# Kernel tuning notes

Measured on AMD Instinct MI355X. Metric: run time of the kernel, lower is better.

Reference implementation:

```python
import jax, jax.numpy as jnp
import numpy as np

L, B, N, D, K = 32, 4, 1000, 128, 8


def setup_inputs() -> dict:
    key = jax.random.key(0)
    ks = jax.random.split(key, 10)
    w = lambda k, s: (jax.random.normal(k, s, jnp.float32) * 0.05)
    return {
        "x": jax.random.normal(ks[0], (L, B, N, D), jnp.float32),
        "route_neighbors": jax.random.randint(ks[1], (N, K), 0, N),
        "t_in_w": w(ks[2], (3 * D, D)),
        "t_in_b": w(ks[3], (3 * D,)),
        "t_out_w": w(ks[4], (D, D)),
        "t_out_b": w(ks[5], (D,)),
        "s_in_w": w(ks[6], (3 * D, D)),
        "s_in_b": w(ks[7], (3 * D,)),
        "s_out_w": w(ks[8], (D, D)),
        "s_out_b": w(ks[9], (D,)),
        "n_heads": 8,
    }


def reference(x, route_neighbors, t_in_w, t_in_b, t_out_w, t_out_b,
              s_in_w, s_in_b, s_out_w, s_out_b, n_heads):
    l, b, n, d = x.shape
    h = n_heads
    dh = d // h
    scale = 1.0 / jnp.sqrt(jnp.asarray(dh, x.dtype))

    # ---- temporal MHA: attend over time axis L, batch = (B, N) ----
    wq, wk, wv = jnp.split(t_in_w, 3, axis=0)
    bq, bk, bv = jnp.split(t_in_b, 3, axis=0)
    q = (x @ wq.T + bq).reshape(l, b, n, h, dh)
    k = (x @ wk.T + bk).reshape(l, b, n, h, dh)
    v = (x @ wv.T + bv).reshape(l, b, n, h, dh)
    scores = jnp.einsum('lbnhd,mbnhd->bnhlm', q, k) * scale
    attn = jax.nn.softmax(scores, axis=-1)
    o = jnp.einsum('bnhlm,mbnhd->lbnhd', attn, v).reshape(l, b, n, d)
    t_out = o @ t_out_w.T + t_out_b

    # ---- spatial MHA: per node, single-token query over K gathered neighbors ----
    swq, swk, swv = jnp.split(s_in_w, 3, axis=0)
    sbq, sbk, sbv = jnp.split(s_in_b, 3, axis=0)
    xn = x[:, :, route_neighbors]                         # (L,B,N,K,D) gather
    sq = (x @ swq.T + sbq).reshape(l, b, n, h, dh)
    sk = (xn @ swk.T + sbk).reshape(l, b, n, -1, h, dh)
    sv = (xn @ swv.T + sbv).reshape(l, b, n, -1, h, dh)
    s_scores = jnp.einsum('lbnhd,lbnkhd->lbnhk', sq, sk) * scale
    s_attn = jax.nn.softmax(s_scores, axis=-1)
    so = jnp.einsum('lbnhk,lbnkhd->lbnhd', s_attn, sv).reshape(l, b, n, d)
    s_out = so @ s_out_w.T + s_out_b

    return t_out + s_out
```

## Files before the change

### kernel.cpp

```cpp
#include <hip/hip_runtime.h>
#include <math.h>

#define L_ 32
#define B_ 4
#define N_ 1000
#define D_ 128
#define H_ 8
#define DH_ 16
#define KN_ 8
#define M_ (L_ * B_ * N_)

typedef __attribute__((ext_vector_type(8))) short short8;
typedef __attribute__((ext_vector_type(8))) unsigned short ushort8v;
typedef __attribute__((ext_vector_type(4))) float floatx4;

static __device__ __forceinline__ unsigned short f2bf(float f) {
  union { float f; unsigned u; } v; v.f = f;
  unsigned r = v.u + 0x7fffu + ((v.u >> 16) & 1u);
  return (unsigned short)(r >> 16);
}
static __device__ __forceinline__ float bf2f(unsigned short s) {
  union { unsigned u; float f; } v; v.u = ((unsigned)s) << 16;
  return v.f;
}
static __device__ __forceinline__ void gload_lds16(const unsigned short* g,
                                                   unsigned short* l) {
  __builtin_amdgcn_global_load_lds(
      (const __attribute__((address_space(1))) unsigned int*)g,
      (__attribute__((address_space(3))) unsigned int*)l, 16, 0, 0);
}

__global__ __launch_bounds__(256) void prep_kernel(
    const float* __restrict__ x, const float* __restrict__ wt_in,
    const float* __restrict__ ws_in, const float* __restrict__ wt_out,
    const float* __restrict__ ws_out, unsigned short* __restrict__ ximg,
    unsigned short* __restrict__ wimg) {
  const int bid = blockIdx.x, t = threadIdx.x;
  const float* src;
  unsigned short* dst;
  if (bid < 1000) {
    src = x + (size_t)bid * 16384;
    dst = ximg + (size_t)bid * 16384;
  } else {
    int w = bid - 1000;
    if (w < 3) src = wt_in + (size_t)w * 16384;
    else if (w < 6) src = ws_in + (size_t)(w - 3) * 16384;
    else if (w == 6) src = wt_out;
    else src = ws_out;
    dst = wimg + (size_t)w * 16384;
  }
#pragma unroll
  for (int it = 0; it < 8; ++it) {
    int gi = it * 256 + t;
    int m = gi >> 4, g = gi & 15;
    const float4* sp = (const float4*)(src + m * 128 + g * 8);
    float4 a = sp[0], b = sp[1];
    ushort8v o;
    o[0] = f2bf(a.x); o[1] = f2bf(a.y); o[2] = f2bf(a.z); o[3] = f2bf(a.w);
    o[4] = f2bf(b.x); o[5] = f2bf(b.y); o[6] = f2bf(b.z); o[7] = f2bf(b.w);
    *(ushort8v*)(dst + (size_t)(m * 16 + (g ^ (m & 7))) * 8) = o;
  }
}

__global__ __launch_bounds__(256) void proj_mfma(
    const unsigned short* __restrict__ ximg,
    const unsigned short* __restrict__ wimg, const float* __restrict__ bias,
    unsigned short* __restrict__ out) {
  __shared__ unsigned short As[128 * 128];
  __shared__ unsigned short Bs[128 * 128];
  const int t = threadIdx.x;
  const int bm = blockIdx.x / 3, bn = blockIdx.x % 3;
  const unsigned short* aSrc = ximg + (size_t)bm * 16384;
  const unsigned short* bSrc = wimg + (size_t)bn * 16384;
#pragma unroll
  for (int it = 0; it < 8; ++it) {
    int gi = it * 256 + t;
    gload_lds16(aSrc + (size_t)gi * 8, &As[gi * 8]);
    gload_lds16(bSrc + (size_t)gi * 8, &Bs[gi * 8]);
  }
  __syncthreads();
  const int wave = t >> 6, lane = t & 63;
  const int wm = (wave >> 1) * 64, wn = (wave & 1) * 64;
  const int lq = lane >> 4, l16 = lane & 15;
  floatx4 acc[4][4] = {};
#pragma unroll
  for (int kk = 0; kk < 4; ++kk) {
    int g = kk * 4 + lq;
    short8 a[4], b[4];
#pragma unroll
    for (int i = 0; i < 4; ++i) {
      int ma = wm + i * 16 + l16;
      a[i] = *(const short8*)(&As[(ma * 16 + (g ^ (ma & 7))) * 8]);
      int nb = wn + i * 16 + l16;
      b[i] = *(const short8*)(&Bs[(nb * 16 + (g ^ (nb & 7))) * 8]);
    }
#pragma unroll
    for (int i = 0; i < 4; ++i)
#pragma unroll
      for (int j = 0; j < 4; ++j)
        acc[i][j] = __builtin_amdgcn_mfma_f32_16x16x32_bf16(a[i], b[j],
                                                            acc[i][j], 0, 0, 0);
  }
  const size_t rowBase = (size_t)bm * 128 + wm;
  const int colBase = bn * 128 + wn;
#pragma unroll
  for (int j = 0; j < 4; ++j) {
    float bb = bias[colBase + j * 16 + l16];
#pragma unroll
    for (int i = 0; i < 4; ++i) {
#pragma unroll
      for (int r = 0; r < 4; ++r) {
        size_t row = rowBase + i * 16 + lq * 4 + r;
        out[row * 384 + colBase + j * 16 + l16] = f2bf(acc[i][j][r] + bb);
      }
    }
  }
}

__global__ __launch_bounds__(256) void tattn_kernel(
    const unsigned short* __restrict__ qkv, unsigned short* __restrict__ oimg) {
  __shared__ unsigned short S[1536 * 8];
  const int t = threadIdx.x;
  const int b = blockIdx.x / N_;
  const int n = blockIdx.x % N_;
  const size_t rowStride = (size_t)B_ * N_ * 384;
  const unsigned short* gbase = qkv + ((size_t)b * N_ + n) * 384;
#pragma unroll
  for (int r = 0; r < 3; ++r) {
#pragma unroll
    for (int it = 0; it < 2; ++it) {
      const int s = it * 256 + t;
      const int m = s >> 4, g = s & 15;
      gload_lds16(gbase + (size_t)m * rowStride + r * 128 + (g ^ (m & 7)) * 8,
                  &S[(r * 512 + s) * 8]);
    }
  }
  asm volatile("s_waitcnt vmcnt(0)" ::: "memory");
  __syncthreads();

  const int wv = t >> 6, lane = t & 63;
  const int lq = lane >> 4, l16 = lane & 15;
  unsigned short* ob[8];
  int rsw[8];
#pragma unroll
  for (int lt = 0; lt < 2; ++lt)
#pragma unroll
    for (int r = 0; r < 4; ++r) {
      const int l = lt * 16 + lq * 4 + r;
      const size_t rg = ((size_t)l * B_ + b) * N_ + n;
      ob[lt * 4 + r] = oimg + (rg >> 7) * 16384 + (size_t)(rg & 127) * 128;
      rsw[lt * 4 + r] = (int)(rg & 7);
    }

#pragma unroll
  for (int hh = 0; hh < 2; ++hh) {
    const int h = wv * 2 + hh;
    short8 ka0 = {}, ka1 = {}, qb0 = {}, qb1 = {};
    if (lq < 2) {
      const int g = 2 * h + lq;
      const int m0 = l16, m1 = 16 + l16;
      ka0 = *(const short8*)&S[(512 + m0 * 16 + (g ^ (m0 & 7))) * 8];
      ka1 = *(const short8*)&S[(512 + m1 * 16 + (g ^ (m1 & 7))) * 8];
      qb0 = *(const short8*)&S[(m0 * 16 + (g ^ (m0 & 7))) * 8];
      qb1 = *(const short8*)&S[(m1 * 16 + (g ^ (m1 & 7))) * 8];
    }
    floatx4 st00 = {}, st01 = {}, st10 = {}, st11 = {};
    st00 = __builtin_amdgcn_mfma_f32_16x16x32_bf16(ka0, qb0, st00, 0, 0, 0);
    st01 = __builtin_amdgcn_mfma_f32_16x16x32_bf16(ka0, qb1, st01, 0, 0, 0);
    st10 = __builtin_amdgcn_mfma_f32_16x16x32_bf16(ka1, qb0, st10, 0, 0, 0);
    st11 = __builtin_amdgcn_mfma_f32_16x16x32_bf16(ka1, qb1, st11, 0, 0, 0);
    const int d = h * 16 + l16;
    const int gd = d >> 3, de = d & 7;
    short8 vb;
#pragma unroll
    for (int j = 0; j < 8; ++j) {
      const int m = ((j >> 2) << 4) + lq * 4 + (j & 3);
      vb[j] = (short)S[(1024 + m * 16 + (gd ^ (m & 7))) * 8 + de];
    }
    short8 pa0, pa1;
    {
      floatx4 a = st00 * 0.25f, c = st10 * 0.25f;
      float mx = fmaxf(fmaxf(fmaxf(a[0], a[1]), fmaxf(a[2], a[3])),
                       fmaxf(fmaxf(c[0], c[1]), fmaxf(c[2], c[3])));
      mx = fmaxf(mx, __shfl_xor(mx, 16));
      mx = fmaxf(mx, __shfl_xor(mx, 32));
      float p0 = __expf(a[0] - mx), p1 = __expf(a[1] - mx);
      float p2 = __expf(a[2] - mx), p3 = __expf(a[3] - mx);
      float p4 = __expf(c[0] - mx), p5 = __expf(c[1] - mx);
      float p6 = __expf(c[2] - mx), p7 = __expf(c[3] - mx);
      float sm = ((p0 + p1) + (p2 + p3)) + ((p4 + p5) + (p6 + p7));
      sm += __shfl_xor(sm, 16);
      sm += __shfl_xor(sm, 32);
      float inv = 1.f / sm;
      pa0[0] = (short)f2bf(p0 * inv); pa0[1] = (short)f2bf(p1 * inv);
      pa0[2] = (short)f2bf(p2 * inv); pa0[3] = (short)f2bf(p3 * inv);
      pa0[4] = (short)f2bf(p4 * inv); pa0[5] = (short)f2bf(p5 * inv);
      pa0[6] = (short)f2bf(p6 * inv); pa0[7] = (short)f2bf(p7 * inv);
    }
    {
      floatx4 a = st01 * 0.25f, c = st11 * 0.25f;
      float mx = fmaxf(fmaxf(fmaxf(a[0], a[1]), fmaxf(a[2], a[3])),
                       fmaxf(fmaxf(c[0], c[1]), fmaxf(c[2], c[3])));
      mx = fmaxf(mx, __shfl_xor(mx, 16));
      mx = fmaxf(mx, __shfl_xor(mx, 32));
      float p0 = __expf(a[0] - mx), p1 = __expf(a[1] - mx);
      float p2 = __expf(a[2] - mx), p3 = __expf(a[3] - mx);
      float p4 = __expf(c[0] - mx), p5 = __expf(c[1] - mx);
      float p6 = __expf(c[2] - mx), p7 = __expf(c[3] - mx);
      float sm = ((p0 + p1) + (p2 + p3)) + ((p4 + p5) + (p6 + p7));
      sm += __shfl_xor(sm, 16);
      sm += __shfl_xor(sm, 32);
      float inv = 1.f / sm;
      pa1[0] = (short)f2bf(p0 * inv); pa1[1] = (short)f2bf(p1 * inv);
      pa1[2] = (short)f2bf(p2 * inv); pa1[3] = (short)f2bf(p3 * inv);
      pa1[4] = (short)f2bf(p4 * inv); pa1[5] = (short)f2bf(p5 * inv);
      pa1[6] = (short)f2bf(p6 * inv); pa1[7] = (short)f2bf(p7 * inv);
    }
    floatx4 o0 = {}, o1 = {};
    o0 = __builtin_amdgcn_mfma_f32_16x16x32_bf16(pa0, vb, o0, 0, 0, 0);
    o1 = __builtin_amdgcn_mfma_f32_16x16x32_bf16(pa1, vb, o1, 0, 0, 0);
#pragma unroll
    for (int r = 0; r < 4; ++r) {
      ob[r][(gd ^ rsw[r]) * 8 + de] = f2bf(o0[r]);
      ob[4 + r][(gd ^ rsw[4 + r]) * 8 + de] = f2bf(o1[r]);
    }
  }
}

__global__ __launch_bounds__(256) void sattn_kernel(
    const unsigned short* __restrict__ qkv, const int* __restrict__ route,
    unsigned short* __restrict__ oimg) {
  const int t = threadIdx.x;
  const int bb = blockIdx.x;
  const int xcd = bb & 7;
  const int idx = bb >> 3;
  const int lb = (idx >> 5) * 8 + xcd;
  const int chunk = idx & 31;
  const int rl = t >> 3, h = t & 7;
  const int nrow = chunk * 32 + rl;
  if (nrow >= N_) return;
  const int n = nrow;
  const int r = lb * N_ + n;
  float q[16];
  {
    const unsigned short* qp = qkv + (size_t)r * 384 + h * DH_;
    ushort8v q0 = *(const ushort8v*)qp;
    ushort8v q1 = *(const ushort8v*)(qp + 8);
#pragma unroll
    for (int i = 0; i < 8; ++i) { q[i] = bf2f(q0[i]); q[8 + i] = bf2f(q1[i]); }
  }
  int nb[KN_];
#pragma unroll
  for (int kk = 0; kk < KN_; ++kk) nb[kk] = route[n * KN_ + kk];
  ushort8v kr[KN_][2], vr[KN_][2];
#pragma unroll
  for (int kk = 0; kk < KN_; ++kk) {
    const unsigned short* base = qkv + ((size_t)lb * N_ + nb[kk]) * 384;
    const unsigned short* kp = base + 128 + h * DH_;
    const unsigned short* vp = base + 256 + h * DH_;
    kr[kk][0] = *(const ushort8v*)kp;
    kr[kk][1] = *(const ushort8v*)(kp + 8);
    vr[kk][0] = *(const ushort8v*)vp;
    vr[kk][1] = *(const ushort8v*)(vp + 8);
  }
  float sc[KN_];
  float mx = -1e30f;
#pragma unroll
  for (int kk = 0; kk < KN_; ++kk) {
    float d = 0.f;
#pragma unroll
    for (int i = 0; i < 8; ++i) {
      d = fmaf(q[i], bf2f(kr[kk][0][i]), d);
      d = fmaf(q[8 + i], bf2f(kr[kk][1][i]), d);
    }
    d *= 0.25f;
    sc[kk] = d;
    mx = fmaxf(mx, d);
  }
  float ssum = 0.f;
#pragma unroll
  for (int kk = 0; kk < KN_; ++kk) { sc[kk] = __expf(sc[kk] - mx); ssum += sc[kk]; }
  float inv = 1.f / ssum;
  float oa[16];
#pragma unroll
  for (int i = 0; i < 16; ++i) oa[i] = 0.f;
#pragma unroll
  for (int kk = 0; kk < KN_; ++kk) {
    float p = sc[kk] * inv;
#pragma unroll
    for (int i = 0; i < 8; ++i) {
      oa[i] = fmaf(p, bf2f(vr[kk][0][i]), oa[i]);
      oa[8 + i] = fmaf(p, bf2f(vr[kk][1][i]), oa[8 + i]);
    }
  }
  ushort8v w0, w1;
#pragma unroll
  for (int i = 0; i < 8; ++i) { w0[i] = f2bf(oa[i]); w1[i] = f2bf(oa[8 + i]); }
  const int m = r & 127;
  unsigned short* base = oimg + (size_t)(r >> 7) * 16384;
  *(ushort8v*)(base + (size_t)(m * 16 + ((2 * h) ^ (m & 7))) * 8) = w0;
  *(ushort8v*)(base + (size_t)(m * 16 + ((2 * h + 1) ^ (m & 7))) * 8) = w1;
}

__global__ __launch_bounds__(256) void final_mfma(
    const unsigned short* __restrict__ otimg,
    const unsigned short* __restrict__ osimg,
    const unsigned short* __restrict__ wtimg,
    const unsigned short* __restrict__ wsimg, const float* __restrict__ bt,
    const float* __restrict__ bs, float* __restrict__ out) {
  __shared__ unsigned short As[128 * 128];
  __shared__ unsigned short Bs[128 * 128];
  const int t = threadIdx.x;
  const int bm = blockIdx.x;
  const int wave = t >> 6, lane = t & 63;
  const int wm = (wave >> 1) * 64, wn = (wave & 1) * 64;
  const int lq = lane >> 4, l16 = lane & 15;
  floatx4 acc[4][4] = {};
#pragma unroll
  for (int p = 0; p < 2; ++p) {
    if (p) __syncthreads();
    const unsigned short* aSrc = (p ? osimg : otimg) + (size_t)bm * 16384;
    const unsigned short* bSrc = p ? wsimg : wtimg;
#pragma unroll
    for (int it = 0; it < 8; ++it) {
      int gi = it * 256 + t;
      gload_lds16(aSrc + (size_t)gi * 8, &As[gi * 8]);
      gload_lds16(bSrc + (size_t)gi * 8, &Bs[gi * 8]);
    }
    __syncthreads();
#pragma unroll
    for (int kk = 0; kk < 4; ++kk) {
      int g = kk * 4 + lq;
      short8 a[4], b[4];
#pragma unroll
      for (int i = 0; i < 4; ++i) {
        int ma = wm + i * 16 + l16;
        a[i] = *(const short8*)(&As[(ma * 16 + (g ^ (ma & 7))) * 8]);
        int nb = wn + i * 16 + l16;
        b[i] = *(const short8*)(&Bs[(nb * 16 + (g ^ (nb & 7))) * 8]);
      }
#pragma unroll
      for (int i = 0; i < 4; ++i)
#pragma unroll
        for (int j = 0; j < 4; ++j)
          acc[i][j] = __builtin_amdgcn_mfma_f32_16x16x32_bf16(a[i], b[j],
                                                              acc[i][j], 0, 0, 0);
    }
  }
  const size_t rowBase = (size_t)bm * 128 + wm;
#pragma unroll
  for (int j = 0; j < 4; ++j) {
    int col = wn + j * 16 + l16;
    float bb = bt[col] + bs[col];
#pragma unroll
    for (int i = 0; i < 4; ++i) {
#pragma unroll
      for (int r = 0; r < 4; ++r) {
        size_t row = rowBase + i * 16 + lq * 4 + r;
        out[row * 128 + col] = acc[i][j][r] + bb;
      }
    }
  }
}

extern "C" void kernel_launch(void* const* d_in, const int* in_sizes, int n_in,
                              void* d_out, int out_size, void* d_ws,
                              size_t ws_size, hipStream_t stream) {
  const float* x = (const float*)d_in[0];
  const int* route = (const int*)d_in[1];
  const float* t_in_w = (const float*)d_in[2];
  const float* t_in_b = (const float*)d_in[3];
  const float* t_out_w = (const float*)d_in[4];
  const float* t_out_b = (const float*)d_in[5];
  const float* s_in_w = (const float*)d_in[6];
  const float* s_in_b = (const float*)d_in[7];
  const float* s_out_w = (const float*)d_in[8];
  const float* s_out_b = (const float*)d_in[9];
  float* out = (float*)d_out;
  unsigned short* ximg = (unsigned short*)d_ws;
  unsigned short* qkv = ximg + (size_t)M_ * 128;
  unsigned short* o_t = qkv + (size_t)M_ * 384;
  unsigned short* wimg = o_t + (size_t)M_ * 128;
  unsigned short* o_s = ximg;

  prep_kernel<<<1008, 256, 0, stream>>>(x, t_in_w, s_in_w, t_out_w, s_out_w,
                                        ximg, wimg);
  proj_mfma<<<(M_ / 128) * 3, 256, 0, stream>>>(ximg, wimg, t_in_b, qkv);
  tattn_kernel<<<B_ * N_, 256, 0, stream>>>(qkv, o_t);
  proj_mfma<<<(M_ / 128) * 3, 256, 0, stream>>>(ximg, wimg + 3 * 16384,
                                                s_in_b, qkv);
  sattn_kernel<<<8 * 16 * 32, 256, 0, stream>>>(qkv, route, o_s);
  final_mfma<<<M_ / 128, 256, 0, stream>>>(o_t, o_s, wimg + 6 * 16384,
                                           wimg + 7 * 16384, t_out_b, s_out_b,
                                           out);
}
```

Measured before the change: 288.7 us.

## Fuse temporal QKV projection into temporal attention kernel

The separate temporal QKV projection GEMM is removed. Each temporal attention block now loads its 32x128 slice of x, computes Q, K and V with MFMA directly against the weights read from global memory, stages Q and K in shared memory, and keeps V in registers. This avoids writing and re-reading the full bf16 QKV buffer for the temporal branch and drops one kernel launch. In exchange each block reads the whole 3x128x128 weight set from global memory or cache rather than through a tiled GEMM, so there is less weight reuse per block.

Result: faster. 267.8 us (-7.2%).

```diff
diff --git a/kernel.cpp b/kernel.cpp
--- a/kernel.cpp
+++ b/kernel.cpp
@@ -117,29 +117,79 @@
   }
 }
 
-__global__ __launch_bounds__(256) void tattn_kernel(
-    const unsigned short* __restrict__ qkv, unsigned short* __restrict__ oimg) {
-  __shared__ unsigned short S[1536 * 8];
+__global__ __launch_bounds__(256) void tattn_fused(
+    const unsigned short* __restrict__ ximg,
+    const unsigned short* __restrict__ wimg,
+    const float* __restrict__ bias,
+    unsigned short* __restrict__ oimg) {
+  __shared__ unsigned short Sx[512 * 8];
+  __shared__ unsigned short Sqk[4][2][32 * 40];
   const int t = threadIdx.x;
   const int b = blockIdx.x / N_;
   const int n = blockIdx.x % N_;
-  const size_t rowStride = (size_t)B_ * N_ * 384;
-  const unsigned short* gbase = qkv + ((size_t)b * N_ + n) * 384;
-#pragma unroll
-  for (int r = 0; r < 3; ++r) {
-#pragma unroll
-    for (int it = 0; it < 2; ++it) {
-      const int s = it * 256 + t;
-      const int m = s >> 4, g = s & 15;
-      gload_lds16(gbase + (size_t)m * rowStride + r * 128 + (g ^ (m & 7)) * 8,
-                  &S[(r * 512 + s) * 8]);
-    }
+  const int c = b * N_ + n;
+#pragma unroll
+  for (int it = 0; it < 2; ++it) {
+    const int s = it * 256 + t;
+    const int ml = s >> 4, gs = s & 15;
+    const int G = gs ^ (ml & 7);
+    const size_t rg = (size_t)ml * (B_ * N_) + c;
+    gload_lds16(ximg + (rg >> 7) * 16384 +
+                    ((rg & 127) * 16 + (size_t)(G ^ ((int)rg & 7))) * 8,
+                &Sx[s * 8]);
   }
   asm volatile("s_waitcnt vmcnt(0)" ::: "memory");
   __syncthreads();
 
   const int wv = t >> 6, lane = t & 63;
   const int lq = lane >> 4, l16 = lane & 15;
+
+  floatx4 aQ[2][2] = {}, aK[2][2] = {}, aV[2][2] = {};
+#pragma unroll
+  for (int kk = 0; kk < 4; ++kk) {
+    short8 a[2];
+#pragma unroll
+    for (int i = 0; i < 2; ++i) {
+      const int ml = i * 16 + l16;
+      a[i] = *(const short8*)&Sx[(ml * 16 + ((kk * 4 + lq) ^ (ml & 7))) * 8];
+    }
+#pragma unroll
+    for (int mat = 0; mat < 3; ++mat) {
+      const unsigned short* wb = wimg + mat * 16384;
+      short8 bf[2];
+#pragma unroll
+      for (int j = 0; j < 2; ++j) {
+        const int nb = wv * 32 + j * 16 + l16;
+        bf[j] =
+            *(const short8*)&wb[(nb * 16 + ((kk * 4 + lq) ^ (nb & 7))) * 8];
+      }
+#pragma unroll
+      for (int i = 0; i < 2; ++i)
+#pragma unroll
+        for (int j = 0; j < 2; ++j) {
+          floatx4* acc = mat == 0 ? &aQ[i][j] : (mat == 1 ? &aK[i][j] : &aV[i][j]);
+          *acc = __builtin_amdgcn_mfma_f32_16x16x32_bf16(a[i], bf[j], *acc, 0,
+                                                         0, 0);
+        }
+    }
+  }
+  const float bQ0 = bias[wv * 32 + l16], bQ1 = bias[wv * 32 + 16 + l16];
+  const float bK0 = bias[128 + wv * 32 + l16],
+              bK1 = bias[128 + wv * 32 + 16 + l16];
+  const float bV0 = bias[256 + wv * 32 + l16],
+              bV1 = bias[256 + wv * 32 + 16 + l16];
+  unsigned short* Sq = Sqk[wv][0];
+  unsigned short* Sk = Sqk[wv][1];
+#pragma unroll
+  for (int i = 0; i < 2; ++i)
+#pragma unroll
+    for (int j = 0; j < 2; ++j)
+#pragma unroll
+      for (int r = 0; r < 4; ++r) {
+        const int m = i * 16 + lq * 4 + r;
+        Sq[m * 40 + j * 16 + l16] = f2bf(aQ[i][j][r] + (j ? bQ1 : bQ0));
+        Sk[m * 40 + j * 16 + l16] = f2bf(aK[i][j][r] + (j ? bK1 : bK0));
+      }
   unsigned short* ob[8];
   int rsw[8];
 #pragma unroll
@@ -147,7 +197,7 @@
 #pragma unroll
     for (int r = 0; r < 4; ++r) {
       const int l = lt * 16 + lq * 4 + r;
-      const size_t rg = ((size_t)l * B_ + b) * N_ + n;
+      const size_t rg = (size_t)l * (B_ * N_) + c;
       ob[lt * 4 + r] = oimg + (rg >> 7) * 16384 + (size_t)(rg & 127) * 128;
       rsw[lt * 4 + r] = (int)(rg & 7);
     }
@@ -157,37 +207,33 @@
     const int h = wv * 2 + hh;
     short8 ka0 = {}, ka1 = {}, qb0 = {}, qb1 = {};
     if (lq < 2) {
-      const int g = 2 * h + lq;
-      const int m0 = l16, m1 = 16 + l16;
-      ka0 = *(const short8*)&S[(512 + m0 * 16 + (g ^ (m0 & 7))) * 8];
-      ka1 = *(const short8*)&S[(512 + m1 * 16 + (g ^ (m1 & 7))) * 8];
-      qb0 = *(const short8*)&S[(m0 * 16 + (g ^ (m0 & 7))) * 8];
-      qb1 = *(const short8*)&S[(m1 * 16 + (g ^ (m1 & 7))) * 8];
+      const int go = (2 * hh + lq) * 8;
+      ka0 = *(const short8*)&Sk[l16 * 40 + go];
+      ka1 = *(const short8*)&Sk[(16 + l16) * 40 + go];
+      qb0 = *(const short8*)&Sq[l16 * 40 + go];
+      qb1 = *(const short8*)&Sq[(16 + l16) * 40 + go];
     }
     floatx4 st00 = {}, st01 = {}, st10 = {}, st11 = {};
     st00 = __builtin_amdgcn_mfma_f32_16x16x32_bf16(ka0, qb0, st00, 0, 0, 0);
     st01 = __builtin_amdgcn_mfma_f32_16x16x32_bf16(ka0, qb1, st01, 0, 0, 0);
     st10 = __builtin_amdgcn_mfma_f32_16x16x32_bf16(ka1, qb0, st10, 0, 0, 0);
     st11 = __builtin_amdgcn_mfma_f32_16x16x32_bf16(ka1, qb1, st11, 0, 0, 0);
-    const int d = h * 16 + l16;
-    const int gd = d >> 3, de = d & 7;
+    const float bV = hh ? bV1 : bV0;
     short8 vb;
 #pragma unroll
-    for (int j = 0; j < 8; ++j) {
-      const int m = ((j >> 2) << 4) + lq * 4 + (j & 3);
-      vb[j] = (short)S[(1024 + m * 16 + (gd ^ (m & 7))) * 8 + de];
-    }
+    for (int j = 0; j < 8; ++j)
+      vb[j] = (short)f2bf(aV[j >> 2][hh][j & 3] + bV);
     short8 pa0, pa1;
     {
-      floatx4 a = st00 * 0.25f, c = st10 * 0.25f;
+      floatx4 a = st00 * 0.25f, cc = st10 * 0.25f;
       float mx = fmaxf(fmaxf(fmaxf(a[0], a[1]), fmaxf(a[2], a[3])),
-                       fmaxf(fmaxf(c[0], c[1]), fmaxf(c[2], c[3])));
+                       fmaxf(fmaxf(cc[0], cc[1]), fmaxf(cc[2], cc[3])));
       mx = fmaxf(mx, __shfl_xor(mx, 16));
       mx = fmaxf(mx, __shfl_xor(mx, 32));
       float p0 = __expf(a[0] - mx), p1 = __expf(a[1] - mx);
       float p2 = __expf(a[2] - mx), p3 = __expf(a[3] - mx);
-      float p4 = __expf(c[0] - mx), p5 = __expf(c[1] - mx);
-      float p6 = __expf(c[2] - mx), p7 = __expf(c[3] - mx);
+      float p4 = __expf(cc[0] - mx), p5 = __expf(cc[1] - mx);
+      float p6 = __expf(cc[2] - mx), p7 = __expf(cc[3] - mx);
       float sm = ((p0 + p1) + (p2 + p3)) + ((p4 + p5) + (p6 + p7));
       sm += __shfl_xor(sm, 16);
       sm += __shfl_xor(sm, 32);
@@ -198,15 +244,15 @@
       pa0[6] = (short)f2bf(p6 * inv); pa0[7] = (short)f2bf(p7 * inv);
     }
     {
-      floatx4 a = st01 * 0.25f, c = st11 * 0.25f;
+      floatx4 a = st01 * 0.25f, cc = st11 * 0.25f;
       float mx = fmaxf(fmaxf(fmaxf(a[0], a[1]), fmaxf(a[2], a[3])),
-                       fmaxf(fmaxf(c[0], c[1]), fmaxf(c[2], c[3])));
+                       fmaxf(fmaxf(cc[0], cc[1]), fmaxf(cc[2], cc[3])));
       mx = fmaxf(mx, __shfl_xor(mx, 16));
       mx = fmaxf(mx, __shfl_xor(mx, 32));
       float p0 = __expf(a[0] - mx), p1 = __expf(a[1] - mx);
       float p2 = __expf(a[2] - mx), p3 = __expf(a[3] - mx);
-      float p4 = __expf(c[0] - mx), p5 = __expf(c[1] - mx);
-      float p6 = __expf(c[2] - mx), p7 = __expf(c[3] - mx);
+      float p4 = __expf(cc[0] - mx), p5 = __expf(cc[1] - mx);
+      float p6 = __expf(cc[2] - mx), p7 = __expf(cc[3] - mx);
       float sm = ((p0 + p1) + (p2 + p3)) + ((p4 + p5) + (p6 + p7));
       sm += __shfl_xor(sm, 16);
       sm += __shfl_xor(sm, 32);
@@ -219,6 +265,8 @@
     floatx4 o0 = {}, o1 = {};
     o0 = __builtin_amdgcn_mfma_f32_16x16x32_bf16(pa0, vb, o0, 0, 0, 0);
     o1 = __builtin_amdgcn_mfma_f32_16x16x32_bf16(pa1, vb, o1, 0, 0, 0);
+    const int d = h * 16 + l16;
+    const int gd = d >> 3, de = d & 7;
 #pragma unroll
     for (int r = 0; r < 4; ++r) {
       ob[r][(gd ^ rsw[r]) * 8 + de] = f2bf(o0[r]);
@@ -385,8 +433,7 @@
 
   prep_kernel<<<1008, 256, 0, stream>>>(x, t_in_w, s_in_w, t_out_w, s_out_w,
                                         ximg, wimg);
-  proj_mfma<<<(M_ / 128) * 3, 256, 0, stream>>>(ximg, wimg, t_in_b, qkv);
-  tattn_kernel<<<B_ * N_, 256, 0, stream>>>(qkv, o_t);
+  tattn_fused<<<B_ * N_, 256, 0, stream>>>(ximg, wimg, t_in_b, o_t);
   proj_mfma<<<(M_ / 128) * 3, 256, 0, stream>>>(ximg, wimg + 3 * 16384,
                                                 s_in_b, qkv);
   sattn_kernel<<<8 * 16 * 32, 256, 0, stream>>>(qkv, route, o_s);
```
